# Kernel tuning notes

Hardware: AMD Instinct MI355X
Metric: run time of the kernel (lower is better)

Reference implementation:

```python
import jax, jax.numpy as jnp
import numpy as np

B, C, H, W = 4, 64, 64, 64
K = C // 8  # conv_f / conv_g output channels (scale=8 since C>=8)


def setup_inputs() -> dict:
    key = jax.random.key(0)
    ks = jax.random.split(key, 8)
    x = jax.random.normal(ks[0], (B, C, H, W), dtype=jnp.float32)
    Wf = jax.random.normal(ks[1], (K, C), dtype=jnp.float32) * 0.05
    bf = jnp.zeros((K,), dtype=jnp.float32)
    Wg = jax.random.normal(ks[2], (K, C), dtype=jnp.float32) * 0.05
    bg = jnp.zeros((K,), dtype=jnp.float32)
    Wh = jax.random.normal(ks[3], (C, C), dtype=jnp.float32) * 0.05
    bh = jnp.zeros((C,), dtype=jnp.float32)
    gamma = jax.random.uniform(ks[4], (1,), dtype=jnp.float32)
    return {"x": x, "Wf": Wf, "bf": bf, "Wg": Wg, "bg": bg,
            "Wh": Wh, "bh": bh, "gamma": gamma}


def reference(x, Wf, bf, Wg, bg, Wh, bh, gamma):
    Bn, Cn, Hn, Wn = x.shape
    HW = Hn * Wn
    xf = x.reshape(Bn, Cn, HW)                               # [B, C, HW]
    # 1x1 convs == per-pixel linear maps over channels
    f = jnp.einsum('kc,bcn->bkn', Wf, xf) + bf[None, :, None]  # [B, K, HW]
    g = jnp.einsum('kc,bcn->bkn', Wg, xf) + bg[None, :, None]  # [B, K, HW]
    h = jnp.einsum('dc,bcn->bdn', Wh, xf) + bh[None, :, None]  # [B, C, HW]
    # s = f^T @ g  -> [B, HW, HW]
    s = jnp.einsum('bki,bkj->bij', f, g)
    # softmax over dim=1 (the first HW axis), matching F.softmax(s, dim=1)
    b = jax.nn.softmax(s, axis=1)
    # post-softmax lower-triangular mask applied to b^T (lower_tri=True)
    tri = jnp.tril(jnp.ones((HW, HW), dtype=x.dtype))
    b_masked = jnp.swapaxes(b, 1, 2) * tri                   # [B, HW, HW]
    o = jnp.einsum('bcn,bnm->bcm', h, b_masked)              # [B, C, HW]
    y = (gamma[0] * o + xf).reshape(Bn, Cn, Hn, Wn)
    return y
```

## Files before the change

kernel.cpp:

```cpp
#include <hip/hip_runtime.h>
#include <hip/hip_bf16.h>

#define HW 4096
#define CC 64
#define NB 4

typedef short bf16x8 __attribute__((ext_vector_type(8)));
typedef short bf16x4 __attribute__((ext_vector_type(4)));
typedef float f32x4 __attribute__((ext_vector_type(4)));

#define OFF_F  0
#define OFF_G  262144
#define OFF_H  524288
#define OFF_ZP 2621440
#define OFF_O  2752512

__device__ __forceinline__ float bf2f(short s) {
    unsigned u = ((unsigned)(unsigned short)s) << 16;
    return __uint_as_float(u);
}
__device__ __forceinline__ __hip_bfloat16 f2bf(float f) { return __float2bfloat16(f); }

__global__ __launch_bounds__(256) void k_prep(
    const float* __restrict__ x,
    const float* __restrict__ Wf, const float* __restrict__ bfv,
    const float* __restrict__ Wg, const float* __restrict__ bgv,
    const float* __restrict__ Wh, const float* __restrict__ bhv,
    __hip_bfloat16* __restrict__ fb, __hip_bfloat16* __restrict__ gb,
    __hip_bfloat16* __restrict__ hb)
{
    __shared__ __align__(16) __hip_bfloat16 xT[64 * 72];
    __shared__ __align__(16) __hip_bfloat16 fgT[64 * 24];

    const int b  = blockIdx.y;
    const int n0 = blockIdx.x * 64;
    const int tid = (int)threadIdx.x;
    const int w = tid >> 6, lane = tid & 63, quad = lane >> 4, l15 = lane & 15;

    {
        const int n = lane;
        const float* xb = x + (size_t)b * (CC * HW) + n0 + n;
#pragma unroll
        for (int i = 0; i < 8; ++i) {
            const int c = (w + 4 * i) * 2;
            const float v0 = xb[(size_t)c * HW];
            const float v1 = xb[(size_t)(c + 1) * HW];
            __hip_bfloat16 t[2] = {f2bf(v0), f2bf(v1)};
            *(unsigned*)&xT[n * 72 + c] = *(const unsigned*)t;
        }
    }

    bf16x8 wa[5][2];
#pragma unroll
    for (int mt = 0; mt < 5; ++mt) {
        const int row = mt * 16 + l15;
        const float* src = (row < 8) ? (Wf + row * 64)
                         : (row < 16) ? (Wg + (row - 8) * 64)
                                      : (Wh + (row - 16) * 64);
#pragma unroll
        for (int kk = 0; kk < 2; ++kk) {
            const float4 a = *(const float4*)(src + kk * 32 + quad * 8);
            const float4 c4 = *(const float4*)(src + kk * 32 + quad * 8 + 4);
            __hip_bfloat16 t[8];
            t[0] = f2bf(a.x);  t[1] = f2bf(a.y);  t[2] = f2bf(a.z);  t[3] = f2bf(a.w);
            t[4] = f2bf(c4.x); t[5] = f2bf(c4.y); t[6] = f2bf(c4.z); t[7] = f2bf(c4.w);
            wa[mt][kk] = *(const bf16x8*)t;
        }
    }

    f32x4 acc[5];
#pragma unroll
    for (int mt = 0; mt < 5; ++mt) {
#pragma unroll
        for (int r = 0; r < 4; ++r) {
            const int grow = mt * 16 + quad * 4 + r;
            acc[mt][r] = (grow < 8) ? bfv[grow]
                       : (grow < 16) ? bgv[grow - 8] : bhv[grow - 16];
        }
    }

    __syncthreads();

    const bf16x8 b0 = *(const bf16x8*)&xT[(w * 16 + l15) * 72 + quad * 8];
    const bf16x8 b1 = *(const bf16x8*)&xT[(w * 16 + l15) * 72 + 32 + quad * 8];
#pragma unroll
    for (int mt = 0; mt < 5; ++mt) {
        acc[mt] = __builtin_amdgcn_mfma_f32_16x16x32_bf16(wa[mt][0], b0, acc[mt], 0, 0, 0);
        acc[mt] = __builtin_amdgcn_mfma_f32_16x16x32_bf16(wa[mt][1], b1, acc[mt], 0, 0, 0);
    }

#pragma unroll
    for (int mt = 1; mt < 5; ++mt) {
#pragma unroll
        for (int r = 0; r < 4; ++r) {
            const int hrow = (mt - 1) * 16 + quad * 4 + r;
            hb[((size_t)(b * 64 + hrow)) * HW + n0 + w * 16 + l15] = f2bf(acc[mt][r]);
        }
    }

#pragma unroll
    for (int r = 0; r < 4; r += 2) {
        __hip_bfloat16 t[2] = {f2bf(acc[0][r]), f2bf(acc[0][r + 1])};
        *(unsigned*)&fgT[(w * 16 + l15) * 24 + quad * 4 + r] = *(const unsigned*)t;
    }
    __syncthreads();
    if (tid < 64) {
        const size_t bn = (size_t)b * HW + n0 + tid;
        *(float4*)(fb + bn * 8) = *(const float4*)&fgT[tid * 24];
    } else if (tid < 128) {
        const int n = tid - 64;
        const size_t bn = (size_t)b * HW + n0 + n;
        *(float4*)(gb + bn * 8) = *(const float4*)&fgT[n * 24 + 8];
    }
}

__global__ __launch_bounds__(256) void k_z(
    const __hip_bfloat16* __restrict__ fb, const __hip_bfloat16* __restrict__ gb,
    float* __restrict__ zp)
{
    __shared__ __align__(16) __hip_bfloat16 fS[2048 * 8];
    __shared__ __align__(16) __hip_bfloat16 gS[64 * 8];
    __shared__ float zred[4][64];

    const int nt = blockIdx.x, b = blockIdx.y, ich = blockIdx.z;
    const int n0 = nt * 64;
    const int tid = (int)threadIdx.x;
    const int w = tid >> 6, lane = tid & 63, quad = lane >> 4, l15 = lane & 15;

    const float4* fsrc = (const float4*)(fb + ((size_t)b * HW + ich * 2048) * 8);
#pragma unroll
    for (int q = 0; q < 8; ++q)
        ((float4*)fS)[q * 256 + tid] = fsrc[q * 256 + tid];
    if (tid < 64)
        *(float4*)&gS[tid * 8] = *(const float4*)(gb + ((size_t)b * HW + n0 + tid) * 8);
    __syncthreads();

    const f32x4 cz = {0.f, 0.f, 0.f, 0.f};
    bf16x8 bgf[4];
#pragma unroll
    for (int ns = 0; ns < 4; ++ns) {
        bf16x8 v = {0, 0, 0, 0, 0, 0, 0, 0};
        if (quad == 0) v = *(const bf16x8*)&gS[(ns * 16 + l15) * 8];
        bgf[ns] = v;
    }

    float z[4] = {0.f, 0.f, 0.f, 0.f};
    bf16x8 cur = {0, 0, 0, 0, 0, 0, 0, 0};
    if (quad == 0) cur = *(const bf16x8*)&fS[(w * 16 + l15) * 8];
    for (int it = 0; it < 32; ++it) {
        bf16x8 nxt = {0, 0, 0, 0, 0, 0, 0, 0};
        if (it + 1 < 32 && quad == 0)
            nxt = *(const bf16x8*)&fS[((it + 1) * 64 + w * 16 + l15) * 8];
#pragma unroll
        for (int ns = 0; ns < 4; ++ns) {
            f32x4 s = __builtin_amdgcn_mfma_f32_16x16x32_bf16(cur, bgf[ns], cz, 0, 0, 0);
            z[ns] += __expf(s[0]) + __expf(s[1]) + __expf(s[2]) + __expf(s[3]);
        }
        cur = nxt;
    }

#pragma unroll
    for (int ns = 0; ns < 4; ++ns) {
        float v = z[ns];
        v += __shfl_xor(v, 16);
        v += __shfl_xor(v, 32);
        if (quad == 0) zred[w][ns * 16 + l15] = v;
    }
    __syncthreads();
    if (tid < 64) {
        float s = zred[0][tid] + zred[1][tid] + zred[2][tid] + zred[3][tid];
        zp[((size_t)ich * NB + b) * HW + n0 + tid] = s;
    }
}

__global__ __launch_bounds__(256) void k_attn(
    const __hip_bfloat16* __restrict__ fb, const __hip_bfloat16* __restrict__ gb,
    const __hip_bfloat16* __restrict__ hb, const float* __restrict__ zp,
    __hip_bfloat16* __restrict__ opart)
{
    __shared__ __align__(16) __hip_bfloat16 gS[64 * 8];
    __shared__ __align__(16) float zS[64];
    __shared__ __align__(16) __hip_bfloat16 hT[64 * 72];
    __shared__ __align__(16) __hip_bfloat16 pT[64 * 72];

    const int hx = blockIdx.x;
    const int b  = blockIdx.y;
    const int r  = blockIdx.z;
    const int mt = (r < 32) ? r : 95 - r;
    const int m0 = mt * 64;
    const int tid = (int)threadIdx.x;
    const int w = tid >> 6, lane = tid & 63, quad = lane >> 4, l15 = lane & 15;

    const int c0s = tid >> 3,         ch0 = tid & 7;
    const int c1s = (256 + tid) >> 3, ch1 = (256 + tid) & 7;

    const f32x4 cz = {0.f, 0.f, 0.f, 0.f};

    bf16x8 af = {0, 0, 0, 0, 0, 0, 0, 0};
    if (quad == 0)
        af = *(const bf16x8*)(fb + ((size_t)b * HW + m0 + w * 16 + l15) * 8);

    f32x4 accO[4];
#pragma unroll
    for (int i = 0; i < 4; ++i) accO[i] = cz;

    const int nc0 = mt + hx;
    float4 hv0 = make_float4(0.f, 0.f, 0.f, 0.f);
    float4 hv1 = hv0, gv = hv0, za = hv0, zb4 = hv0;
    if (nc0 < 64) {
        const int n1 = nc0 * 64;
        hv0 = *(const float4*)(hb + ((size_t)(b * 64 + c0s)) * HW + n1 + ch0 * 8);
        hv1 = *(const float4*)(hb + ((size_t)(b * 64 + c1s)) * HW + n1 + ch1 * 8);
        if (tid < 64) gv = *(const float4*)(gb + ((size_t)b * HW + n1 + tid) * 8);
        else if (tid < 80) {
            const int j4 = (tid - 64) * 4;
            za  = *(const float4*)(zp + (size_t)b * HW + n1 + j4);
            zb4 = *(const float4*)(zp + ((size_t)NB + b) * HW + n1 + j4);
        }
    }

    for (int nc = nc0; nc < 64; nc += 2) {
        __syncthreads();
        *(float4*)&hT[c0s * 72 + ch0 * 8] = hv0;
        *(float4*)&hT[c1s * 72 + ch1 * 8] = hv1;
        if (tid < 64) *(float4*)&gS[tid * 8] = gv;
        else if (tid < 80) {
            float4 zi;
            zi.x = 1.f / (za.x + zb4.x);
            zi.y = 1.f / (za.y + zb4.y);
            zi.z = 1.f / (za.z + zb4.z);
            zi.w = 1.f / (za.w + zb4.w);
            *(float4*)&zS[(tid - 64) * 4] = zi;
        }
        const int nn = nc + 2;
        if (nn < 64) {
            const int n1 = nn * 64;
            hv0 = *(const float4*)(hb + ((size_t)(b * 64 + c0s)) * HW + n1 + ch0 * 8);
            hv1 = *(const float4*)(hb + ((size_t)(b * 64 + c1s)) * HW + n1 + ch1 * 8);
            if (tid < 64) gv = *(const float4*)(gb + ((size_t)b * HW + n1 + tid) * 8);
            else if (tid < 80) {
                const int j4 = (tid - 64) * 4;
                za  = *(const float4*)(zp + (size_t)b * HW + n1 + j4);
                zb4 = *(const float4*)(zp + ((size_t)NB + b) * HW + n1 + j4);
            }
        }
        __syncthreads();

        const int n0c = nc * 64;
        const bool diag = (nc == mt);
#pragma unroll
        for (int ns = 0; ns < 4; ++ns) {
            bf16x8 bg2 = {0, 0, 0, 0, 0, 0, 0, 0};
            if (quad == 0) bg2 = *(const bf16x8*)&gS[(ns * 16 + l15) * 8];
            f32x4 s = __builtin_amdgcn_mfma_f32_16x16x32_bf16(bg2, af, cz, 0, 0, 0);
            const float4 zi4 = *(const float4*)&zS[ns * 16 + quad * 4];
            __hip_bfloat16 t4[4];
#pragma unroll
            for (int j = 0; j < 4; ++j) {
                float p = __expf(s[j]) * ((const float*)&zi4)[j];
                if (diag) {
                    const int n = n0c + ns * 16 + quad * 4 + j;
                    const int m = m0 + w * 16 + l15;
                    if (n < m) p = 0.f;
                }
                t4[j] = f2bf(p);
            }
            *(bf16x4*)&pT[(w * 16 + l15) * 72 + ns * 16 + quad * 4] = *(const bf16x4*)t4;
        }
#pragma unroll
        for (int kb = 0; kb < 2; ++kb) {
            const bf16x8 ap =
                *(const bf16x8*)&pT[(w * 16 + l15) * 72 + kb * 32 + quad * 8];
#pragma unroll
            for (int cs = 0; cs < 4; ++cs) {
                const bf16x8 bh2 =
                    *(const bf16x8*)&hT[(cs * 16 + l15) * 72 + kb * 32 + quad * 8];
                accO[cs] = __builtin_amdgcn_mfma_f32_16x16x32_bf16(ap, bh2, accO[cs], 0, 0, 0);
            }
        }
    }

#pragma unroll
    for (int cs = 0; cs < 4; ++cs) {
        const int c = cs * 16 + l15;
        __hip_bfloat16 tmp[4];
#pragma unroll
        for (int j = 0; j < 4; ++j) tmp[j] = f2bf(accO[cs][j]);
        *(float2*)(opart + ((size_t)((hx * NB + b) * 64 + c)) * HW + m0 + w * 16 + quad * 4) =
            *(const float2*)tmp;
    }
}

__global__ __launch_bounds__(256) void k_epi(
    const __hip_bfloat16* __restrict__ opart, const float* __restrict__ x,
    const float* __restrict__ gamma, float* __restrict__ y)
{
    const int t = blockIdx.x * 256 + (int)threadIdx.x;
    const size_t e0 = (size_t)t * 8;
    const float ga = gamma[0];

    float acc[8] = {0, 0, 0, 0, 0, 0, 0, 0};
#pragma unroll
    for (int h = 0; h < 2; ++h) {
        const bf16x8 v = *(const bf16x8*)(opart + (size_t)h * (NB * CC * HW) + e0);
#pragma unroll
        for (int k = 0; k < 8; ++k) acc[k] += bf2f(v[k]);
    }
    const float4 x0 = *(const float4*)(x + e0);
    const float4 x1 = *(const float4*)(x + e0 + 4);
    float4 y0, y1;
    y0.x = ga * acc[0] + x0.x; y0.y = ga * acc[1] + x0.y;
    y0.z = ga * acc[2] + x0.z; y0.w = ga * acc[3] + x0.w;
    y1.x = ga * acc[4] + x1.x; y1.y = ga * acc[5] + x1.y;
    y1.z = ga * acc[6] + x1.z; y1.w = ga * acc[7] + x1.w;
    *(float4*)(y + e0) = y0;
    *(float4*)(y + e0 + 4) = y1;
}

extern "C" void kernel_launch(void* const* d_in, const int* in_sizes, int n_in,
                              void* d_out, int out_size, void* d_ws, size_t ws_size,
                              hipStream_t stream)
{
    const float* x     = (const float*)d_in[0];
    const float* Wf    = (const float*)d_in[1];
    const float* bfv   = (const float*)d_in[2];
    const float* Wg    = (const float*)d_in[3];
    const float* bgv   = (const float*)d_in[4];
    const float* Wh    = (const float*)d_in[5];
    const float* bhv   = (const float*)d_in[6];
    const float* gamma = (const float*)d_in[7];

    char* ws = (char*)d_ws;
    __hip_bfloat16* fb = (__hip_bfloat16*)(ws + OFF_F);
    __hip_bfloat16* gb = (__hip_bfloat16*)(ws + OFF_G);
    __hip_bfloat16* hb = (__hip_bfloat16*)(ws + OFF_H);
    float* zp          = (float*)(ws + OFF_ZP);
    __hip_bfloat16* opart = (__hip_bfloat16*)(ws + OFF_O);
    float* y = (float*)d_out;

    k_prep<<<dim3(64, 4), 256, 0, stream>>>(x, Wf, bfv, Wg, bgv, Wh, bhv, fb, gb, hb);
    k_z<<<dim3(64, 4, 2), 256, 0, stream>>>(fb, gb, zp);
    k_attn<<<dim3(2, 4, 64), 256, 0, stream>>>(fb, gb, hb, zp, opart);
    k_epi<<<512, 256, 0, stream>>>(opart, x, gamma, y);
}
```

Baseline: 127.5 us.

## Pair mirrored row tiles per attention block and split column sweep eight ways

The attention kernel now gives each block two mirrored query row tiles (mtA and 63-mtA). Each loaded h/g/z column tile is reused for both, and the causal column range is split into 8 interleaved partitions instead of 2, which balances the triangular work and raises the block count. The prep kernel moves to 32-pixel blocks with strips spread across waves, giving it more parallelism and writing f/g directly without the extra LDS pass. In exchange there are 8 bf16 partial outputs, so the epilogue reads four times more partial data and the workspace grows.

```diff
diff --git a/kernel.cpp b/kernel.cpp
--- a/kernel.cpp
+++ b/kernel.cpp
@@ -29,89 +29,75 @@
     __hip_bfloat16* __restrict__ fb, __hip_bfloat16* __restrict__ gb,
     __hip_bfloat16* __restrict__ hb)
 {
-    __shared__ __align__(16) __hip_bfloat16 xT[64 * 72];
-    __shared__ __align__(16) __hip_bfloat16 fgT[64 * 24];
+    __shared__ __align__(16) __hip_bfloat16 xS[32 * 72];
 
     const int b  = blockIdx.y;
-    const int n0 = blockIdx.x * 64;
+    const int n0 = blockIdx.x * 32;
     const int tid = (int)threadIdx.x;
     const int w = tid >> 6, lane = tid & 63, quad = lane >> 4, l15 = lane & 15;
 
     {
-        const int n = lane;
-        const float* xb = x + (size_t)b * (CC * HW) + n0 + n;
-#pragma unroll
-        for (int i = 0; i < 8; ++i) {
-            const int c = (w + 4 * i) * 2;
-            const float v0 = xb[(size_t)c * HW];
-            const float v1 = xb[(size_t)(c + 1) * HW];
-            __hip_bfloat16 t[2] = {f2bf(v0), f2bf(v1)};
-            *(unsigned*)&xT[n * 72 + c] = *(const unsigned*)t;
-        }
-    }
-
-    bf16x8 wa[5][2];
-#pragma unroll
-    for (int mt = 0; mt < 5; ++mt) {
-        const int row = mt * 16 + l15;
+        const int px = tid & 31, c0 = (tid >> 5) * 8;
+        const float* xb = x + (size_t)b * (CC * HW) + n0 + px;
+        float xv[8];
+#pragma unroll
+        for (int k = 0; k < 8; ++k) xv[k] = xb[(size_t)(c0 + k) * HW];
+#pragma unroll
+        for (int k = 0; k < 8; k += 2) {
+            __hip_bfloat16 t2[2] = {f2bf(xv[k]), f2bf(xv[k + 1])};
+            *(unsigned*)&xS[px * 72 + c0 + k] = *(const unsigned*)t2;
+        }
+    }
+    __syncthreads();
+
+    const int pxg = w & 1, grp = w >> 1;
+    const int p = n0 + pxg * 16 + l15;
+    const bf16x8 xb0 = *(const bf16x8*)&xS[(pxg * 16 + l15) * 72 + quad * 8];
+    const bf16x8 xb1 = *(const bf16x8*)&xS[(pxg * 16 + l15) * 72 + 32 + quad * 8];
+
+    auto do_strip = [&](int s) {
+        const int row = s * 16 + l15;
         const float* src = (row < 8) ? (Wf + row * 64)
                          : (row < 16) ? (Wg + (row - 8) * 64)
                                       : (Wh + (row - 16) * 64);
+        bf16x8 wa[2];
 #pragma unroll
         for (int kk = 0; kk < 2; ++kk) {
-            const float4 a = *(const float4*)(src + kk * 32 + quad * 8);
-            const float4 c4 = *(const float4*)(src + kk * 32 + quad * 8 + 4);
-            __hip_bfloat16 t[8];
-            t[0] = f2bf(a.x);  t[1] = f2bf(a.y);  t[2] = f2bf(a.z);  t[3] = f2bf(a.w);
-            t[4] = f2bf(c4.x); t[5] = f2bf(c4.y); t[6] = f2bf(c4.z); t[7] = f2bf(c4.w);
-            wa[mt][kk] = *(const bf16x8*)t;
-        }
-    }
-
-    f32x4 acc[5];
-#pragma unroll
-    for (int mt = 0; mt < 5; ++mt) {
-#pragma unroll
-        for (int r = 0; r < 4; ++r) {
-            const int grow = mt * 16 + quad * 4 + r;
-            acc[mt][r] = (grow < 8) ? bfv[grow]
-                       : (grow < 16) ? bgv[grow - 8] : bhv[grow - 16];
-        }
-    }
-
-    __syncthreads();
-
-    const bf16x8 b0 = *(const bf16x8*)&xT[(w * 16 + l15) * 72 + quad * 8];
-    const bf16x8 b1 = *(const bf16x8*)&xT[(w * 16 + l15) * 72 + 32 + quad * 8];
-#pragma unroll
-    for (int mt = 0; mt < 5; ++mt) {
-        acc[mt] = __builtin_amdgcn_mfma_f32_16x16x32_bf16(wa[mt][0], b0, acc[mt], 0, 0, 0);
-        acc[mt] = __builtin_amdgcn_mfma_f32_16x16x32_bf16(wa[mt][1], b1, acc[mt], 0, 0, 0);
-    }
-
-#pragma unroll
-    for (int mt = 1; mt < 5; ++mt) {
-#pragma unroll
-        for (int r = 0; r < 4; ++r) {
-            const int hrow = (mt - 1) * 16 + quad * 4 + r;
-            hb[((size_t)(b * 64 + hrow)) * HW + n0 + w * 16 + l15] = f2bf(acc[mt][r]);
-        }
-    }
-
-#pragma unroll
-    for (int r = 0; r < 4; r += 2) {
-        __hip_bfloat16 t[2] = {f2bf(acc[0][r]), f2bf(acc[0][r + 1])};
-        *(unsigned*)&fgT[(w * 16 + l15) * 24 + quad * 4 + r] = *(const unsigned*)t;
-    }
-    __syncthreads();
-    if (tid < 64) {
-        const size_t bn = (size_t)b * HW + n0 + tid;
-        *(float4*)(fb + bn * 8) = *(const float4*)&fgT[tid * 24];
-    } else if (tid < 128) {
-        const int n = tid - 64;
-        const size_t bn = (size_t)b * HW + n0 + n;
-        *(float4*)(gb + bn * 8) = *(const float4*)&fgT[n * 24 + 8];
-    }
+            const float4 a4 = *(const float4*)(src + kk * 32 + quad * 8);
+            const float4 b4 = *(const float4*)(src + kk * 32 + quad * 8 + 4);
+            __hip_bfloat16 t8[8];
+            t8[0] = f2bf(a4.x); t8[1] = f2bf(a4.y); t8[2] = f2bf(a4.z); t8[3] = f2bf(a4.w);
+            t8[4] = f2bf(b4.x); t8[5] = f2bf(b4.y); t8[6] = f2bf(b4.z); t8[7] = f2bf(b4.w);
+            wa[kk] = *(const bf16x8*)t8;
+        }
+        f32x4 acc;
+#pragma unroll
+        for (int rr = 0; rr < 4; ++rr) {
+            const int grow = s * 16 + quad * 4 + rr;
+            acc[rr] = (grow < 8) ? bfv[grow]
+                    : (grow < 16) ? bgv[grow - 8] : bhv[grow - 16];
+        }
+        acc = __builtin_amdgcn_mfma_f32_16x16x32_bf16(wa[0], xb0, acc, 0, 0, 0);
+        acc = __builtin_amdgcn_mfma_f32_16x16x32_bf16(wa[1], xb1, acc, 0, 0, 0);
+        if (s == 0) {
+            const size_t bn = (size_t)b * HW + p;
+            __hip_bfloat16* base = (quad < 2 ? fb : gb) + bn * 8 + (quad & 1) * 4;
+            __hip_bfloat16 t2[2];
+            t2[0] = f2bf(acc[0]); t2[1] = f2bf(acc[1]);
+            *(unsigned*)&base[0] = *(const unsigned*)t2;
+            t2[0] = f2bf(acc[2]); t2[1] = f2bf(acc[3]);
+            *(unsigned*)&base[2] = *(const unsigned*)t2;
+        } else {
+#pragma unroll
+            for (int rr = 0; rr < 4; ++rr) {
+                const int hrow = (s - 1) * 16 + quad * 4 + rr;
+                hb[((size_t)(b * 64 + hrow)) * HW + p] = f2bf(acc[rr]);
+            }
+        }
+    };
+    do_strip(grp ? 2 : 0);
+    do_strip(grp ? 3 : 1);
+    if (!grp) do_strip(4);
 }
 
 __global__ __launch_bounds__(256) void k_z(
@@ -183,11 +169,11 @@
     __shared__ __align__(16) __hip_bfloat16 hT[64 * 72];
     __shared__ __align__(16) __hip_bfloat16 pT[64 * 72];
 
-    const int hx = blockIdx.x;
-    const int b  = blockIdx.y;
-    const int r  = blockIdx.z;
-    const int mt = (r < 32) ? r : 95 - r;
-    const int m0 = mt * 64;
+    const int hx  = blockIdx.x;
+    const int b   = blockIdx.y;
+    const int mtA = blockIdx.z;
+    const int mtB = 63 - mtA;
+    const int m0A = mtA * 64, m0B = mtB * 64;
     const int tid = (int)threadIdx.x;
     const int w = tid >> 6, lane = tid & 63, quad = lane >> 4, l15 = lane & 15;
 
@@ -196,18 +182,21 @@
 
     const f32x4 cz = {0.f, 0.f, 0.f, 0.f};
 
-    bf16x8 af = {0, 0, 0, 0, 0, 0, 0, 0};
-    if (quad == 0)
-        af = *(const bf16x8*)(fb + ((size_t)b * HW + m0 + w * 16 + l15) * 8);
-
-    f32x4 accO[4];
-#pragma unroll
-    for (int i = 0; i < 4; ++i) accO[i] = cz;
-
-    const int nc0 = mt + hx;
+    bf16x8 afA = {0, 0, 0, 0, 0, 0, 0, 0}, afB = afA;
+    if (quad == 0) {
+        afA = *(const bf16x8*)(fb + ((size_t)b * HW + m0A + w * 16 + l15) * 8);
+        afB = *(const bf16x8*)(fb + ((size_t)b * HW + m0B + w * 16 + l15) * 8);
+    }
+
+    f32x4 accA[4], accB[4];
+#pragma unroll
+    for (int i = 0; i < 4; ++i) { accA[i] = cz; accB[i] = cz; }
+
+    const int nc0 = mtA + (((hx - (mtA & 7)) + 8) & 7);
+
     float4 hv0 = make_float4(0.f, 0.f, 0.f, 0.f);
     float4 hv1 = hv0, gv = hv0, za = hv0, zb4 = hv0;
-    if (nc0 < 64) {
+    {
         const int n1 = nc0 * 64;
         hv0 = *(const float4*)(hb + ((size_t)(b * 64 + c0s)) * HW + n1 + ch0 * 8);
         hv1 = *(const float4*)(hb + ((size_t)(b * 64 + c1s)) * HW + n1 + ch1 * 8);
@@ -219,7 +208,7 @@
         }
     }
 
-    for (int nc = nc0; nc < 64; nc += 2) {
+    for (int nc = nc0; nc < 64; nc += 8) {
         __syncthreads();
         *(float4*)&hT[c0s * 72 + ch0 * 8] = hv0;
         *(float4*)&hT[c1s * 72 + ch1 * 8] = hv1;
@@ -232,7 +221,7 @@
             zi.w = 1.f / (za.w + zb4.w);
             *(float4*)&zS[(tid - 64) * 4] = zi;
         }
-        const int nn = nc + 2;
+        const int nn = nc + 8;
         if (nn < 64) {
             const int n1 = nn * 64;
             hv0 = *(const float4*)(hb + ((size_t)(b * 64 + c0s)) * HW + n1 + ch0 * 8);
@@ -247,35 +236,67 @@
         __syncthreads();
 
         const int n0c = nc * 64;
-        const bool diag = (nc == mt);
-#pragma unroll
-        for (int ns = 0; ns < 4; ++ns) {
-            bf16x8 bg2 = {0, 0, 0, 0, 0, 0, 0, 0};
-            if (quad == 0) bg2 = *(const bf16x8*)&gS[(ns * 16 + l15) * 8];
-            f32x4 s = __builtin_amdgcn_mfma_f32_16x16x32_bf16(bg2, af, cz, 0, 0, 0);
-            const float4 zi4 = *(const float4*)&zS[ns * 16 + quad * 4];
-            __hip_bfloat16 t4[4];
-#pragma unroll
-            for (int j = 0; j < 4; ++j) {
-                float p = __expf(s[j]) * ((const float*)&zi4)[j];
-                if (diag) {
-                    const int n = n0c + ns * 16 + quad * 4 + j;
-                    const int m = m0 + w * 16 + l15;
-                    if (n < m) p = 0.f;
+
+        {
+            const bool diag = (nc == mtA);
+#pragma unroll
+            for (int ns = 0; ns < 4; ++ns) {
+                bf16x8 bg2 = {0, 0, 0, 0, 0, 0, 0, 0};
+                if (quad == 0) bg2 = *(const bf16x8*)&gS[(ns * 16 + l15) * 8];
+                f32x4 s = __builtin_amdgcn_mfma_f32_16x16x32_bf16(bg2, afA, cz, 0, 0, 0);
+                const float4 zi4 = *(const float4*)&zS[ns * 16 + quad * 4];
+                __hip_bfloat16 t4[4];
+#pragma unroll
+                for (int j = 0; j < 4; ++j) {
+                    float p = __expf(s[j]) * ((const float*)&zi4)[j];
+                    if (diag) {
+                        const int n = n0c + ns * 16 + quad * 4 + j;
+                        const int m = m0A + w * 16 + l15;
+                        if (n < m) p = 0.f;
+                    }
+                    t4[j] = f2bf(p);
                 }
-                t4[j] = f2bf(p);
-            }
-            *(bf16x4*)&pT[(w * 16 + l15) * 72 + ns * 16 + quad * 4] = *(const bf16x4*)t4;
-        }
-#pragma unroll
-        for (int kb = 0; kb < 2; ++kb) {
-            const bf16x8 ap =
-                *(const bf16x8*)&pT[(w * 16 + l15) * 72 + kb * 32 + quad * 8];
-#pragma unroll
-            for (int cs = 0; cs < 4; ++cs) {
-                const bf16x8 bh2 =
-                    *(const bf16x8*)&hT[(cs * 16 + l15) * 72 + kb * 32 + quad * 8];
-                accO[cs] = __builtin_amdgcn_mfma_f32_16x16x32_bf16(ap, bh2, accO[cs], 0, 0, 0);
+                *(bf16x4*)&pT[(w * 16 + l15) * 72 + ns * 16 + quad * 4] = *(const bf16x4*)t4;
+            }
+#pragma unroll
+            for (int kb = 0; kb < 2; ++kb) {
+                const bf16x8 ap = *(const bf16x8*)&pT[(w * 16 + l15) * 72 + kb * 32 + quad * 8];
+#pragma unroll
+                for (int cs = 0; cs < 4; ++cs) {
+                    const bf16x8 bh2 = *(const bf16x8*)&hT[(cs * 16 + l15) * 72 + kb * 32 + quad * 8];
+                    accA[cs] = __builtin_amdgcn_mfma_f32_16x16x32_bf16(ap, bh2, accA[cs], 0, 0, 0);
+                }
+            }
+        }
+        if (nc >= mtB) {
+            const bool diag = (nc == mtB);
+#pragma unroll
+            for (int ns = 0; ns < 4; ++ns) {
+                bf16x8 bg2 = {0, 0, 0, 0, 0, 0, 0, 0};
+                if (quad == 0) bg2 = *(const bf16x8*)&gS[(ns * 16 + l15) * 8];
+                f32x4 s = __builtin_amdgcn_mfma_f32_16x16x32_bf16(bg2, afB, cz, 0, 0, 0);
+                const float4 zi4 = *(const float4*)&zS[ns * 16 + quad * 4];
+                __hip_bfloat16 t4[4];
+#pragma unroll
+                for (int j = 0; j < 4; ++j) {
+                    float p = __expf(s[j]) * ((const float*)&zi4)[j];
+                    if (diag) {
+                        const int n = n0c + ns * 16 + quad * 4 + j;
+                        const int m = m0B + w * 16 + l15;
+                        if (n < m) p = 0.f;
+                    }
+                    t4[j] = f2bf(p);
+                }
+                *(bf16x4*)&pT[(w * 16 + l15) * 72 + ns * 16 + quad * 4] = *(const bf16x4*)t4;
+            }
+#pragma unroll
+            for (int kb = 0; kb < 2; ++kb) {
+                const bf16x8 ap = *(const bf16x8*)&pT[(w * 16 + l15) * 72 + kb * 32 + quad * 8];
+#pragma unroll
+                for (int cs = 0; cs < 4; ++cs) {
+                    const bf16x8 bh2 = *(const bf16x8*)&hT[(cs * 16 + l15) * 72 + kb * 32 + quad * 8];
+                    accB[cs] = __builtin_amdgcn_mfma_f32_16x16x32_bf16(ap, bh2, accB[cs], 0, 0, 0);
+                }
             }
         }
     }
@@ -283,11 +304,12 @@
 #pragma unroll
     for (int cs = 0; cs < 4; ++cs) {
         const int c = cs * 16 + l15;
-        __hip_bfloat16 tmp[4];
-#pragma unroll
-        for (int j = 0; j < 4; ++j) tmp[j] = f2bf(accO[cs][j]);
-        *(float2*)(opart + ((size_t)((hx * NB + b) * 64 + c)) * HW + m0 + w * 16 + quad * 4) =
-            *(const float2*)tmp;
+        __hip_bfloat16 tA[4], tB[4];
+#pragma unroll
+        for (int j = 0; j < 4; ++j) { tA[j] = f2bf(accA[cs][j]); tB[j] = f2bf(accB[cs][j]); }
+        const size_t base = ((size_t)((hx * NB + b) * 64 + c)) * HW;
+        *(float2*)(opart + base + m0A + w * 16 + quad * 4) = *(const float2*)tA;
+        *(float2*)(opart + base + m0B + w * 16 + quad * 4) = *(const float2*)tB;
     }
 }
 
@@ -301,7 +323,7 @@
 
     float acc[8] = {0, 0, 0, 0, 0, 0, 0, 0};
 #pragma unroll
-    for (int h = 0; h < 2; ++h) {
+    for (int h = 0; h < 8; ++h) {
         const bf16x8 v = *(const bf16x8*)(opart + (size_t)h * (NB * CC * HW) + e0);
 #pragma unroll
         for (int k = 0; k < 8; ++k) acc[k] += bf2f(v[k]);
@@ -338,8 +360,8 @@
     __hip_bfloat16* opart = (__hip_bfloat16*)(ws + OFF_O);
     float* y = (float*)d_out;
 
-    k_prep<<<dim3(64, 4), 256, 0, stream>>>(x, Wf, bfv, Wg, bgv, Wh, bhv, fb, gb, hb);
+    k_prep<<<dim3(128, 4), 256, 0, stream>>>(x, Wf, bfv, Wg, bgv, Wh, bhv, fb, gb, hb);
     k_z<<<dim3(64, 4, 2), 256, 0, stream>>>(fb, gb, zp);
-    k_attn<<<dim3(2, 4, 64), 256, 0, stream>>>(fb, gb, hb, zp, opart);
+    k_attn<<<dim3(8, 4, 32), 256, 0, stream>>>(fb, gb, hb, zp, opart);
     k_epi<<<512, 256, 0, stream>>>(opart, x, gamma, y);
 }
```

New measurement: 121.0 us. -5.1%, faster.
